# Optimization experiments

Hardware: AMD Instinct MI355X
Metric: run time of the kernel (lower is better)

## Reference

```python
import jax, jax.numpy as jnp
import numpy as np

N_HEAD, D_EMB, D_MLP, D_HEAD = 12, 768, 3072, 64
LN_EPS = 1e-5


def setup_inputs() -> dict:
    key = jax.random.key(0)
    ks = jax.random.split(key, 12)
    s = 0.02
    return {
        "x": jax.random.normal(ks[0], (2, 4096, D_EMB), dtype=jnp.float32),
        "ln1_g": jnp.ones((D_EMB,), jnp.float32),
        "ln1_b": jnp.zeros((D_EMB,), jnp.float32),
        "wqkv_w": jax.random.normal(ks[1], (D_EMB, 3 * D_EMB), jnp.float32) * s,
        "wo_w": jax.random.normal(ks[2], (D_EMB, D_EMB), jnp.float32) * s,
        "wo_b": jnp.zeros((D_EMB,), jnp.float32),
        "ln2_g": jnp.ones((D_EMB,), jnp.float32),
        "ln2_b": jnp.zeros((D_EMB,), jnp.float32),
        "w1_w": jax.random.normal(ks[3], (D_EMB, D_MLP), jnp.float32) * s,
        "w1_b": jnp.zeros((D_MLP,), jnp.float32),
        "w2_w": jax.random.normal(ks[4], (D_MLP, D_EMB), jnp.float32) * s,
        "w2_b": jnp.zeros((D_EMB,), jnp.float32),
    }


def _layernorm(x, g, b):
    mu = jnp.mean(x, axis=-1, keepdims=True)
    var = jnp.var(x, axis=-1, keepdims=True)
    return (x - mu) * jax.lax.rsqrt(var + LN_EPS) * g + b


def _attn(x, wqkv_w, wo_w, wo_b):
    B, T, d = x.shape
    qkv = x @ wqkv_w  # [B,T,3d]
    q, k, v = jnp.split(qkv, 3, axis=-1)
    q = q.reshape(B, T, N_HEAD, D_HEAD).transpose(0, 2, 1, 3)  # [B,H,T,dh]
    k = k.reshape(B, T, N_HEAD, D_HEAD).transpose(0, 2, 1, 3)
    v = v.reshape(B, T, N_HEAD, D_HEAD).transpose(0, 2, 1, 3)
    A = jnp.einsum('bhqd,bhkd->bhqk', q, k) / np.sqrt(D_HEAD).astype(np.float32)
    mask = jnp.tril(jnp.ones((T, T), dtype=bool))
    A = jnp.where(mask, A, -jnp.inf)
    A = jax.nn.softmax(A - jax.lax.stop_gradient(jnp.max(A, axis=-1, keepdims=True)), axis=-1)
    y = jnp.einsum('bhqk,bhkd->bhqd', A, v)  # [B,H,T,dh]
    y = y.transpose(0, 2, 1, 3).reshape(B, T, d)
    return y @ wo_w + wo_b


def _mlp(x, w1_w, w1_b, w2_w, w2_b):
    h = jax.nn.gelu(x @ w1_w + w1_b, approximate=False)
    return h @ w2_w + w2_b


def reference(x, ln1_g, ln1_b, wqkv_w, wo_w, wo_b, ln2_g, ln2_b, w1_w, w1_b, w2_w, w2_b):
    x = x + _attn(_layernorm(x, ln1_g, ln1_b), wqkv_w, wo_w, wo_b)
    x = x + _mlp(_layernorm(x, ln2_g, ln2_b), w1_w, w1_b, w2_w, w2_b)
    return x
```

## Files before the change

kernel.cpp:

```cpp
#include <hip/hip_runtime.h>

#define T_SEQ 4096
#define D_EMB 768
#define N_HEAD 12
#define D_HEAD 64
#define D_MLP 3072
#define NTOK 8192
#define QSCALE 0.18033688011112043f

typedef __bf16 v8bf __attribute__((ext_vector_type(8)));
typedef float v4f __attribute__((ext_vector_type(4)));
typedef short v4s __attribute__((ext_vector_type(4)));
typedef unsigned v2u __attribute__((ext_vector_type(2)));

template <int N> struct IC { static constexpr int value = N; };

__device__ __forceinline__ unsigned short f2bf(float f) {
    unsigned int u = __float_as_uint(f);
    unsigned int r = (u + 0x7fffu + ((u >> 16) & 1u)) >> 16;
    return (unsigned short)r;
}

__device__ __forceinline__ void g2lds16(const void* g, void* l) {
    __builtin_amdgcn_global_load_lds(
        (const __attribute__((address_space(1))) void*)g,
        (__attribute__((address_space(3))) void*)l, 16, 0, 0);
}

__device__ __forceinline__ float fastrcp(float x) {
#if __has_builtin(__builtin_amdgcn_rcpf)
    return __builtin_amdgcn_rcpf(x);
#else
    return 1.f / x;
#endif
}

__device__ __forceinline__ void pl32swap(unsigned& a, unsigned& b) {
#if __has_builtin(__builtin_amdgcn_permlane32_swap)
    v2u r = __builtin_amdgcn_permlane32_swap(a, b, false, false);
    a = r[0]; b = r[1];
#else
    asm volatile("v_permlane32_swap_b32 %0, %1" : "+v"(a), "+v"(b));
#endif
}
__device__ __forceinline__ void pl16swap(unsigned& a, unsigned& b) {
#if __has_builtin(__builtin_amdgcn_permlane16_swap)
    v2u r = __builtin_amdgcn_permlane16_swap(a, b, false, false);
    a = r[0]; b = r[1];
#else
    asm volatile("v_permlane16_swap_b32 %0, %1" : "+v"(a), "+v"(b));
#endif
}

__device__ __forceinline__ int sg(int r) { return (r ^ (r >> 2)) & 3; }

__global__ void tcast_kernel(const float* __restrict__ in, unsigned short* __restrict__ out,
                             int K, int N) {
    __shared__ float tile[32][33];
    int k0 = blockIdx.y * 32, n0 = blockIdx.x * 32;
    int tx = threadIdx.x, ty = threadIdx.y;
    for (int i = ty; i < 32; i += 8)
        tile[i][tx] = in[(size_t)(k0 + i) * N + n0 + tx];
    __syncthreads();
    for (int i = ty; i < 32; i += 8)
        out[(size_t)(n0 + i) * K + k0 + tx] = f2bf(tile[tx][i]);
}

__global__ void vtrans_kernel(const unsigned short* __restrict__ in,
                              unsigned short* __restrict__ out) {
    __shared__ unsigned short tile[32][33];
    size_t base = (size_t)blockIdx.z * T_SEQ * D_HEAD;
    int t0 = blockIdx.x * 32, d0 = blockIdx.y * 32;
    int tx = threadIdx.x, ty = threadIdx.y;
    for (int i = ty; i < 32; i += 8)
        tile[i][tx] = in[base + (size_t)(t0 + i) * D_HEAD + d0 + tx];
    __syncthreads();
    size_t tbase = base + (size_t)(t0 >> 6) * 4096 + (t0 & 32);
    for (int i = ty; i < 32; i += 8)
        out[tbase + (size_t)(d0 + i) * 64 + tx] = tile[tx][i];
}

__global__ __launch_bounds__(256) void ln_kernel(const float* __restrict__ x,
                                                 const float* __restrict__ g,
                                                 const float* __restrict__ bta,
                                                 unsigned short* __restrict__ out) {
    int row = blockIdx.x;
    const float* xr = x + (size_t)row * D_EMB;
    int tid = threadIdx.x;
    float v[3];
    float s = 0.f, s2 = 0.f;
#pragma unroll
    for (int i = 0; i < 3; i++) {
        v[i] = xr[tid + i * 256];
        s += v[i];
        s2 += v[i] * v[i];
    }
#pragma unroll
    for (int o = 1; o < 64; o <<= 1) {
        s += __shfl_xor(s, o);
        s2 += __shfl_xor(s2, o);
    }
    __shared__ float red[8];
    int wave = tid >> 6, lane = tid & 63;
    if (lane == 0) { red[wave] = s; red[wave + 4] = s2; }
    __syncthreads();
    s = red[0] + red[1] + red[2] + red[3];
    s2 = red[4] + red[5] + red[6] + red[7];
    float mu = s * (1.f / 768.f);
    float var = s2 * (1.f / 768.f) - mu * mu;
    float rstd = rsqrtf(var + 1e-5f);
#pragma unroll
    for (int i = 0; i < 3; i++) {
        int c = tid + i * 256;
        out[(size_t)row * D_EMB + c] = f2bf((v[i] - mu) * rstd * g[c] + bta[c]);
    }
}

template <int EPI, int MT>
__global__ __launch_bounds__(256) void gemm_kernel(
    const unsigned short* __restrict__ A, const unsigned short* __restrict__ Bt, int K,
    int Nt, const float* __restrict__ bias, const float* __restrict__ resid,
    float* __restrict__ outF, unsigned short* __restrict__ outB,
    unsigned short* __restrict__ Qb, unsigned short* __restrict__ Kb,
    unsigned short* __restrict__ Vb) {
    constexpr int NAI = (MT == 128) ? 4 : 2;
    __shared__ unsigned short As[2][MT * 32];
    __shared__ unsigned short Bs[2][4096];
    const int tid = threadIdx.x;
    const int wave = tid >> 6, lane = tid & 63;
    const int n16 = lane & 15, kq = lane >> 4;
    const int moff = (wave >> 1) * (MT / 2), noff = (wave & 1) * 64;
    const int id = blockIdx.x;
    const int xcd = id & 7, s = id >> 3;
    const int mt = xcd * (NTOK / MT / 8) + s / Nt, nt_ = s % Nt;
    const long m0 = (long)mt * MT, nb0 = (long)nt_ * 128;

    const int c0 = (wave * 2 + 0) * 64 + lane;
    const int c1 = (wave * 2 + 1) * 64 + lane;
    const int r0 = c0 >> 2, r1 = c1 >> 2;
    const unsigned short* bP0 = Bt + (nb0 + r0) * K + (((c0 & 3) ^ sg(r0)) << 3);
    const unsigned short* bP1 = Bt + (nb0 + r1) * K + (((c1 & 3) ^ sg(r1)) << 3);
    const int ca = (MT == 128) ? c0 : (wave * 64 + lane);
    const int ra = ca >> 2;
    const unsigned short* aP0 = A + (m0 + ra) * K + (((ca & 3) ^ sg(ra)) << 3);
    const unsigned short* aP1 = (MT == 128)
        ? A + (m0 + r1) * K + (((c1 & 3) ^ sg(r1)) << 3) : nullptr;
    const int sn = sg(n16);
    const int fw = (noff + n16) * 32 + ((kq ^ sn) << 3);
    const int fa = (moff + n16) * 32 + ((kq ^ sn) << 3);

    const v4f vzero = {0.f, 0.f, 0.f, 0.f};
    v4f acc[4][NAI];
#pragma unroll
    for (int wi = 0; wi < 4; wi++)
#pragma unroll
        for (int ai = 0; ai < NAI; ai++) acc[wi][ai] = vzero;

    auto stage = [&](auto BUFC, int kpos) {
        constexpr int nb = decltype(BUFC)::value;
        if (MT == 128) {
            g2lds16(aP0 + kpos, &As[nb][(wave * 2 + 0) * 512]);
            g2lds16(aP1 + kpos, &As[nb][(wave * 2 + 1) * 512]);
        } else {
            g2lds16(aP0 + kpos, &As[nb][wave * 512]);
        }
        g2lds16(bP0 + kpos, &Bs[nb][(wave * 2 + 0) * 512]);
        g2lds16(bP1 + kpos, &Bs[nb][(wave * 2 + 1) * 512]);
    };
    auto gstep = [&](auto BUFC, int kpos, bool pref) {
        constexpr int buf = decltype(BUFC)::value;
        __syncthreads();
        if (pref) stage(IC<buf ^ 1>{}, kpos + 32);
        v8bf wf[4], af[NAI];
#pragma unroll
        for (int i = 0; i < 4; i++) wf[i] = *(const v8bf*)(&Bs[buf][fw + i * 512]);
#pragma unroll
        for (int i = 0; i < NAI; i++) af[i] = *(const v8bf*)(&As[buf][fa + i * 512]);
#pragma unroll
        for (int wi = 0; wi < 4; wi++)
#pragma unroll
            for (int ai = 0; ai < NAI; ai++)
                acc[wi][ai] = __builtin_amdgcn_mfma_f32_16x16x32_bf16(wf[wi], af[ai],
                                                                     acc[wi][ai], 0, 0, 0);
    };

    stage(IC<0>{}, 0);
#pragma unroll 1
    for (int k0 = 0; k0 < K; k0 += 64) {
        gstep(IC<0>{}, k0, true);
        gstep(IC<1>{}, k0 + 32, k0 + 64 < K);
    }

#pragma unroll
    for (int wi = 0; wi < 4; wi++) {
#pragma unroll
        for (int ai = 0; ai < NAI; ai++) {
            const long Nb = nb0 + noff + wi * 16 + kq * 4;
            const long M = m0 + moff + ai * 16 + n16;
            if (EPI == 0) {
                int which = (int)(Nb / 768);
                int c = (int)(Nb - which * 768);
                int hh = c >> 6, ii = c & 63;
                int bb = (int)(M >> 12), t = (int)(M & 4095);
                size_t dst = (((size_t)bb * N_HEAD + hh) * T_SEQ + t) * D_HEAD + ii;
                union { uint2 u2; unsigned short us[4]; } pk;
#pragma unroll
                for (int r = 0; r < 4; r++) {
                    float v = acc[wi][ai][r];
                    if (which == 0) v *= QSCALE;
                    pk.us[r] = f2bf(v);
                }
                if (which == 0) *(uint2*)(&Qb[dst]) = pk.u2;
                else if (which == 1) *(uint2*)(&Kb[dst]) = pk.u2;
                else *(uint2*)(&Vb[dst]) = pk.u2;
            } else if (EPI == 1) {
                float4 b4 = *(const float4*)(&bias[Nb]);
                float4 r4 = *(const float4*)(&resid[M * 768 + Nb]);
                float4 o4;
                o4.x = acc[wi][ai][0] + b4.x + r4.x;
                o4.y = acc[wi][ai][1] + b4.y + r4.y;
                o4.z = acc[wi][ai][2] + b4.z + r4.z;
                o4.w = acc[wi][ai][3] + b4.w + r4.w;
                *(float4*)(&outF[M * 768 + Nb]) = o4;
            } else {
                float4 b4 = *(const float4*)(&bias[Nb]);
                union { uint2 u2; unsigned short us[4]; } pk;
#pragma unroll
                for (int r = 0; r < 4; r++) {
                    float t = acc[wi][ai][r] + ((const float*)&b4)[r];
                    float y = t * (-2.302118131f + t * t * -0.1029433585f);
                    float gl = t * fastrcp(1.f + __builtin_amdgcn_exp2f(y));
                    pk.us[r] = f2bf(gl);
                }
                *(uint2*)(&outB[M * 3072 + Nb]) = pk.u2;
            }
        }
    }
}

__global__ __launch_bounds__(256) void attn_kernel(const unsigned short* __restrict__ Q,
                                                   const unsigned short* __restrict__ Kg,
                                                   const unsigned short* __restrict__ Vt,
                                                   unsigned short* __restrict__ y) {
    __shared__ unsigned short Kt[2][4096];
    __shared__ unsigned short Vl[2][4096];
    const int tid = threadIdx.x;
    const int wave = tid >> 6, lane = tid & 63;
    const int n16 = lane & 15, kq = lane >> 4;
    const int id = blockIdx.x;
    const int xcd = id & 7, slot = id >> 3;
    const int combo = xcd * 3 + (slot % 3);
    const int qt = 63 - slot / 3;
    const int h = combo % N_HEAD, b = combo / N_HEAD;
    const size_t hoff = (((size_t)b * N_HEAD + h) * T_SEQ) * D_HEAD;
    const unsigned short* Qh = Q + hoff;
    const unsigned short* Kh = Kg + hoff;
    const unsigned short* Vh = Vt + hoff;
    const v4f vzero = {0.f, 0.f, 0.f, 0.f};

    const int sC0 = (wave * 2 + 0) * 64 + lane;
    const int sC1 = (wave * 2 + 1) * 64 + lane;
    const int soff0 = (sC0 >> 3) * 64 + ((((sC0 & 7) ^ ((sC0 >> 3) & 7))) << 3);
    const int soff1 = (sC1 >> 3) * 64 + ((((sC1 & 7) ^ ((sC1 >> 3) & 7))) << 3);
    const int fb0 = n16 * 64 + ((kq ^ (n16 & 7)) << 3);
    const int fb1 = n16 * 64 + (((4 + kq) ^ (n16 & 7)) << 3);
    v8bf vone;
#pragma unroll
    for (int j = 0; j < 8; j++) ((unsigned short*)&vone)[j] = 0x3F80;

    const int qglob = qt * 64 + wave * 16 + n16;
    v8bf qf[2];
#pragma unroll
    for (int ks = 0; ks < 2; ks++)
        qf[ks] = *(const v8bf*)(&Qh[(size_t)qglob * D_HEAD + ks * 32 + kq * 8]);

    v4f o[4], lacc;
#pragma unroll
    for (int nt = 0; nt < 4; nt++) o[nt] = vzero;
    lacc = vzero;

    const unsigned short* knext;
    const unsigned short* vnext;

    auto step = [&](auto BUFC, int kt, bool pref, bool diag) {
        constexpr int buf = decltype(BUFC)::value;
        __syncthreads();
        if (pref) {
            g2lds16(knext + soff0, &Kt[buf ^ 1][(wave * 2 + 0) * 512]);
            g2lds16(knext + soff1, &Kt[buf ^ 1][(wave * 2 + 1) * 512]);
            g2lds16(vnext + soff0, &Vl[buf ^ 1][(wave * 2 + 0) * 512]);
            g2lds16(vnext + soff1, &Vl[buf ^ 1][(wave * 2 + 1) * 512]);
            knext += 4096;
            vnext += 4096;
        }
        v4f s[4];
#pragma unroll
        for (int nt = 0; nt < 4; nt++) s[nt] = vzero;
        __builtin_amdgcn_s_setprio(1);
#pragma unroll
        for (int nt = 0; nt < 4; nt++) {
            v8bf k0 = *(const v8bf*)(&Kt[buf][nt * 1024 + fb0]);
            v8bf k1 = *(const v8bf*)(&Kt[buf][nt * 1024 + fb1]);
            s[nt] = __builtin_amdgcn_mfma_f32_16x16x32_bf16(k0, qf[0], s[nt], 0, 0, 0);
            s[nt] = __builtin_amdgcn_mfma_f32_16x16x32_bf16(k1, qf[1], s[nt], 0, 0, 0);
        }
        __builtin_amdgcn_s_setprio(0);
        union PW { v4s s4; unsigned u[2]; } pa[4];
#pragma unroll
        for (int ntk = 0; ntk < 4; ntk++) {
            union { v4s s4; __bf16 h[4]; } pk;
#pragma unroll
            for (int r = 0; r < 4; r++) {
                float p = __builtin_amdgcn_exp2f(s[ntk][r]);
                if (diag) {
                    int key = kt * 64 + ntk * 16 + kq * 4 + r;
                    if (key > qglob) p = 0.f;
                }
                pk.h[r] = (__bf16)p;
            }
            pa[ntk].s4 = pk.s4;
        }
        union F8 { v8bf v; unsigned u[4]; } pf[2];
#pragma unroll
        for (int ks = 0; ks < 2; ks++) {
#pragma unroll
            for (int j = 0; j < 2; j++) {
                unsigned X = pa[2 * ks].u[j], Y = pa[2 * ks + 1].u[j];
                pl32swap(X, Y);
                pl16swap(X, Y);
                pf[ks].u[j] = X;
                pf[ks].u[j + 2] = Y;
            }
        }
        __builtin_amdgcn_s_setprio(1);
#pragma unroll
        for (int ks = 0; ks < 2; ks++) {
            lacc = __builtin_amdgcn_mfma_f32_16x16x32_bf16(pf[ks].v, vone, lacc, 0, 0, 0);
#pragma unroll
            for (int nt = 0; nt < 4; nt++) {
                v8bf vb = *(const v8bf*)(&Vl[buf][nt * 1024 + (ks ? fb1 : fb0)]);
                o[nt] = __builtin_amdgcn_mfma_f32_16x16x32_bf16(pf[ks].v, vb, o[nt], 0, 0, 0);
            }
        }
        __builtin_amdgcn_s_setprio(0);
    };

    g2lds16(Kh + soff0, &Kt[0][(wave * 2 + 0) * 512]);
    g2lds16(Kh + soff1, &Kt[0][(wave * 2 + 1) * 512]);
    g2lds16(Vh + soff0, &Vl[0][(wave * 2 + 0) * 512]);
    g2lds16(Vh + soff1, &Vl[0][(wave * 2 + 1) * 512]);
    knext = Kh + 4096;
    vnext = Vh + 4096;

    int kt = 0;
#pragma unroll 1
    while (kt + 2 <= qt) {
        step(IC<0>{}, kt, true, false);
        step(IC<1>{}, kt + 1, true, false);
        kt += 2;
    }
    if (kt < qt) {
        step(IC<0>{}, kt, true, false);
        step(IC<1>{}, kt + 1, false, true);
    } else {
        step(IC<0>{}, kt, false, true);
    }

    float linv[4];
#pragma unroll
    for (int r = 0; r < 4; r++) linv[r] = fastrcp(lacc[r]);
#pragma unroll
    for (int nt = 0; nt < 4; nt++)
#pragma unroll
        for (int r = 0; r < 4; r++) {
            int q = qt * 64 + wave * 16 + kq * 4 + r;
            float val = o[nt][r] * linv[r];
            y[((size_t)b * T_SEQ + q) * D_EMB + h * 64 + nt * 16 + n16] = f2bf(val);
        }
}

extern "C" void kernel_launch(void* const* d_in, const int* in_sizes, int n_in,
                              void* d_out, int out_size, void* d_ws, size_t ws_size,
                              hipStream_t stream) {
    const float* x = (const float*)d_in[0];
    const float* ln1_g = (const float*)d_in[1];
    const float* ln1_b = (const float*)d_in[2];
    const float* wqkv_w = (const float*)d_in[3];
    const float* wo_w = (const float*)d_in[4];
    const float* wo_b = (const float*)d_in[5];
    const float* ln2_g = (const float*)d_in[6];
    const float* ln2_b = (const float*)d_in[7];
    const float* w1_w = (const float*)d_in[8];
    const float* w1_b = (const float*)d_in[9];
    const float* w2_w = (const float*)d_in[10];
    const float* w2_b = (const float*)d_in[11];
    float* out = (float*)d_out;

    char* ws = (char*)d_ws;
    size_t off = 0;
    auto alloc = [&](size_t bytes) -> void* {
        void* p = ws + off;
        off += (bytes + 255) & ~(size_t)255;
        return p;
    };
    unsigned short* xn = (unsigned short*)alloc((size_t)NTOK * D_EMB * 2);
    unsigned short* wqkvT = (unsigned short*)alloc((size_t)2304 * 768 * 2);
    unsigned short* woT = (unsigned short*)alloc((size_t)768 * 768 * 2);
    unsigned short* w1T = (unsigned short*)alloc((size_t)3072 * 768 * 2);
    unsigned short* w2T = (unsigned short*)alloc((size_t)768 * 3072 * 2);
    unsigned short* Qb = (unsigned short*)alloc((size_t)NTOK * D_EMB * 2);
    unsigned short* Kb = (unsigned short*)alloc((size_t)NTOK * D_EMB * 2);
    unsigned short* Vb = (unsigned short*)alloc((size_t)NTOK * D_EMB * 2);
    unsigned short* yb = (unsigned short*)alloc((size_t)NTOK * D_EMB * 2);
    float* res1 = (float*)alloc((size_t)NTOK * D_EMB * 4);
    unsigned short* Vtb = xn;
    unsigned short* hbuf = Qb;

    dim3 tb(32, 8);
    tcast_kernel<<<dim3(2304 / 32, 768 / 32), tb, 0, stream>>>(wqkv_w, wqkvT, 768, 2304);
    tcast_kernel<<<dim3(768 / 32, 768 / 32), tb, 0, stream>>>(wo_w, woT, 768, 768);
    tcast_kernel<<<dim3(3072 / 32, 768 / 32), tb, 0, stream>>>(w1_w, w1T, 768, 3072);
    tcast_kernel<<<dim3(768 / 32, 3072 / 32), tb, 0, stream>>>(w2_w, w2T, 3072, 768);

    ln_kernel<<<NTOK, 256, 0, stream>>>(x, ln1_g, ln1_b, xn);

    gemm_kernel<0, 128><<<1152, 256, 0, stream>>>(
        xn, wqkvT, 768, 18, nullptr, nullptr, nullptr, nullptr, Qb, Kb, Vb);

    vtrans_kernel<<<dim3(T_SEQ / 32, 2, 2 * N_HEAD), tb, 0, stream>>>(Vb, Vtb);

    attn_kernel<<<1536, 256, 0, stream>>>(Qb, Kb, Vtb, yb);

    gemm_kernel<1, 128><<<384, 256, 0, stream>>>(
        yb, woT, 768, 6, wo_b, x, res1, nullptr, nullptr, nullptr, nullptr);

    ln_kernel<<<NTOK, 256, 0, stream>>>(res1, ln2_g, ln2_b, xn);

    gemm_kernel<2, 128><<<1536, 256, 0, stream>>>(
        xn, w1T, 768, 24, w1_b, nullptr, nullptr, hbuf, nullptr, nullptr, nullptr);

    gemm_kernel<1, 128><<<384, 256, 0, stream>>>(
        hbuf, w2T, 3072, 6, w2_b, res1, out, nullptr, nullptr, nullptr, nullptr);
}
```

Before: 426.3 us.

## Use intra-block split-K GEMM for the two N=768 residual projections

Adds a 512-thread GEMM kernel in which two groups of four waves each compute half of the K dimension for the same 128x128 output tile. The partial sums are then combined through shared memory before the bias and residual epilogue. It replaces the 256-thread kernel for the output projection and the MLP down-projection, which launch only 384 blocks. The aim is more waves in flight per tile to hide latency on these under-filled GEMMs, at the cost of an extra LDS reduction and a larger shared-memory footprint per block.

```diff
diff --git a/kernel.cpp b/kernel.cpp
--- a/kernel.cpp
+++ b/kernel.cpp
@@ -238,6 +238,108 @@
     }
 }
 
+__global__ __launch_bounds__(512, 4) void gemm_splitk_kernel(
+    const unsigned short* __restrict__ A, const unsigned short* __restrict__ Bt, int K,
+    int Nt, const float* __restrict__ bias, const float* __restrict__ resid,
+    float* __restrict__ outF) {
+    __shared__ __align__(16) unsigned short SH[32768];
+    const int tid = threadIdx.x;
+    const int wave = tid >> 6, lane = tid & 63;
+    const int kg = wave >> 2, wv = wave & 3;
+    const int n16 = lane & 15, kq = lane >> 4;
+    const int moff = (wv >> 1) * 64, noff = (wv & 1) * 64;
+    const int id = blockIdx.x;
+    const int xcd = id & 7, s = id >> 3;
+    const int mt = xcd * (NTOK / 128 / 8) + s / Nt, nt_ = s % Nt;
+    const long m0 = (long)mt * 128, nb0 = (long)nt_ * 128;
+    const int Kh = K >> 1;
+
+    const int c0 = (wv * 2 + 0) * 64 + lane;
+    const int c1 = (wv * 2 + 1) * 64 + lane;
+    const int r0 = c0 >> 2, r1 = c1 >> 2;
+    const int kb = kg * Kh;
+    const unsigned short* bP0 = Bt + (nb0 + r0) * K + ((((c0 & 3) ^ sg(r0)) << 3) + kb);
+    const unsigned short* bP1 = Bt + (nb0 + r1) * K + ((((c1 & 3) ^ sg(r1)) << 3) + kb);
+    const unsigned short* aP0 = A + (m0 + r0) * K + ((((c0 & 3) ^ sg(r0)) << 3) + kb);
+    const unsigned short* aP1 = A + (m0 + r1) * K + ((((c1 & 3) ^ sg(r1)) << 3) + kb);
+    const int sn = sg(n16);
+    const int fw = (noff + n16) * 32 + ((kq ^ sn) << 3);
+    const int fa = (moff + n16) * 32 + ((kq ^ sn) << 3);
+    const int abase = kg * 8192, bbase = 16384 + kg * 8192;
+
+    const v4f vzero = {0.f, 0.f, 0.f, 0.f};
+    v4f acc[4][4];
+#pragma unroll
+    for (int wi = 0; wi < 4; wi++)
+#pragma unroll
+        for (int ai = 0; ai < 4; ai++) acc[wi][ai] = vzero;
+
+    auto stage = [&](auto BUFC, int kpos) {
+        constexpr int nb = decltype(BUFC)::value;
+        unsigned short* asb = SH + abase + nb * 4096;
+        unsigned short* bsb = SH + bbase + nb * 4096;
+        g2lds16(aP0 + kpos, asb + (wv * 2 + 0) * 512);
+        g2lds16(aP1 + kpos, asb + (wv * 2 + 1) * 512);
+        g2lds16(bP0 + kpos, bsb + (wv * 2 + 0) * 512);
+        g2lds16(bP1 + kpos, bsb + (wv * 2 + 1) * 512);
+    };
+    auto gstep = [&](auto BUFC, int kpos, bool pref) {
+        constexpr int buf = decltype(BUFC)::value;
+        __syncthreads();
+        if (pref) stage(IC<buf ^ 1>{}, kpos + 32);
+        const unsigned short* asb = SH + abase + buf * 4096;
+        const unsigned short* bsb = SH + bbase + buf * 4096;
+        v8bf wf[4], af[4];
+#pragma unroll
+        for (int i = 0; i < 4; i++) wf[i] = *(const v8bf*)(bsb + fw + i * 512);
+#pragma unroll
+        for (int i = 0; i < 4; i++) af[i] = *(const v8bf*)(asb + fa + i * 512);
+#pragma unroll
+        for (int wi = 0; wi < 4; wi++)
+#pragma unroll
+            for (int ai = 0; ai < 4; ai++)
+                acc[wi][ai] = __builtin_amdgcn_mfma_f32_16x16x32_bf16(wf[wi], af[ai],
+                                                                     acc[wi][ai], 0, 0, 0);
+    };
+
+    stage(IC<0>{}, 0);
+#pragma unroll 1
+    for (int k0 = 0; k0 < Kh; k0 += 64) {
+        gstep(IC<0>{}, k0, true);
+        gstep(IC<1>{}, k0 + 32, k0 + 64 < Kh);
+    }
+
+    __syncthreads();
+    v4f* ex = (v4f*)SH;
+    if (kg == 1) {
+#pragma unroll
+        for (int wi = 0; wi < 4; wi++)
+#pragma unroll
+            for (int ai = 0; ai < 4; ai++)
+                ex[((wv * 16 + wi * 4 + ai) << 6) + lane] = acc[wi][ai];
+    }
+    __syncthreads();
+    if (kg == 1) return;
+
+#pragma unroll
+    for (int wi = 0; wi < 4; wi++) {
+#pragma unroll
+        for (int ai = 0; ai < 4; ai++) {
+            v4f p = ex[((wv * 16 + wi * 4 + ai) << 6) + lane];
+            const long Nb = nb0 + noff + wi * 16 + kq * 4;
+            const long M = m0 + moff + ai * 16 + n16;
+            float4 b4 = *(const float4*)(&bias[Nb]);
+            float4 r4 = *(const float4*)(&resid[M * 768 + Nb]);
+            float4 o4;
+            o4.x = acc[wi][ai][0] + p[0] + b4.x + r4.x;
+            o4.y = acc[wi][ai][1] + p[1] + b4.y + r4.y;
+            o4.z = acc[wi][ai][2] + p[2] + b4.z + r4.z;
+            o4.w = acc[wi][ai][3] + p[3] + b4.w + r4.w;
+            *(float4*)(&outF[M * 768 + Nb]) = o4;
+        }
+    }
+}
+
 __global__ __launch_bounds__(256) void attn_kernel(const unsigned short* __restrict__ Q,
                                                    const unsigned short* __restrict__ Kg,
                                                    const unsigned short* __restrict__ Vt,
@@ -431,14 +533,14 @@
 
     attn_kernel<<<1536, 256, 0, stream>>>(Qb, Kb, Vtb, yb);
 
-    gemm_kernel<1, 128><<<384, 256, 0, stream>>>(
-        yb, woT, 768, 6, wo_b, x, res1, nullptr, nullptr, nullptr, nullptr);
+    gemm_splitk_kernel<<<384, 512, 0, stream>>>(
+        yb, woT, 768, 6, wo_b, x, res1);
 
     ln_kernel<<<NTOK, 256, 0, stream>>>(res1, ln2_g, ln2_b, xn);
 
     gemm_kernel<2, 128><<<1536, 256, 0, stream>>>(
         xn, w1T, 768, 24, w1_b, nullptr, nullptr, hbuf, nullptr, nullptr, nullptr);
 
-    gemm_kernel<1, 128><<<384, 256, 0, stream>>>(
-        hbuf, w2T, 3072, 6, w2_b, res1, out, nullptr, nullptr, nullptr, nullptr);
-}
+    gemm_splitk_kernel<<<384, 512, 0, stream>>>(
+        hbuf, w2T, 3072, 6, w2_b, res1, out);
+}
```

Measured after the change: 412.5 us. -3.3%, faster.
